# Kernel tuning notes

Hardware: AMD Instinct MI355X
Metric: run time of the kernel (lower is better)

Reference implementation:

```python
import jax, jax.numpy as jnp
import numpy as np

HIDDEN = 1024
NUM_HEADS = 8
HEAD_DIM = HIDDEN // NUM_HEADS
MAX_BACKWARD = 11   # context_left - 1
MAX_FORWARD = 12    # context_right
SPAN = MAX_BACKWARD + MAX_FORWARD + 1  # 24

B, U, W, C = 8, 16, 128, 151


def setup_inputs() -> dict:
    key = jax.random.key(0)
    kq, kk, kp = jax.random.split(key, 3)
    queries = jax.random.normal(kq, (B, U, W, NUM_HEADS, HEAD_DIM), dtype=jnp.float32)
    keys = jax.random.normal(kk, (B, U, C, NUM_HEADS, HEAD_DIM), dtype=jnp.float32)
    # glorot-ish scale for pos_proj (hidden, num_heads*head_dim)
    pos_proj = jax.random.normal(kp, (HIDDEN, NUM_HEADS * HEAD_DIM), dtype=jnp.float32) * (1.0 / np.sqrt(HIDDEN))
    return {"queries": queries, "keys": keys, "pos_proj": pos_proj}


def _sinusoid_emb(pos_proj):
    # positions: max_backward .. -max_forward (descending), shape (SPAN,)
    pos = jnp.arange(MAX_BACKWARD, -(MAX_FORWARD + 1), -1, dtype=jnp.float32)
    num_ts = HIDDEN // 2
    inv_ts = jnp.ones((num_ts,), dtype=jnp.float32)  # module uses ones
    scaled = pos[:, None] * inv_ts[None, :]          # (SPAN, HIDDEN/2)
    signal = jnp.concatenate([jnp.sin(scaled), jnp.cos(scaled)], axis=-1)  # (SPAN, HIDDEN)
    proj = signal @ pos_proj                         # (SPAN, N*H)
    return proj.reshape(SPAN, NUM_HEADS, HEAD_DIM)


def _relative_shift(term_bd, context_size):
    # term_bd: (B, N, U, W, SPAN) -> (B, N, U, W, C)
    b, n, u, w, _ = term_bd.shape
    pad = context_size + 1 - SPAN
    padded = jnp.pad(term_bd, ((0, 0), (0, 0), (0, 0), (0, 0), (0, pad)))
    flat = padded.reshape(b, n, u, w * (context_size + 1))
    sliced = flat[:, :, :, : w * context_size]
    return sliced.reshape(b, n, u, w, context_size)


def reference(queries, keys, pos_proj):
    context_size = keys.shape[2]
    sin_emb = _sinusoid_emb(pos_proj)                      # (SPAN, N, H)
    qp = jnp.transpose(queries, (0, 3, 1, 2, 4))           # (B, N, U, W, H)
    kp = jnp.transpose(keys, (0, 3, 1, 4, 2))              # (B, N, U, H, C)
    term_ac = jnp.matmul(qp, kp)                           # (B, N, U, W, C)
    # term_bd: query-position interaction, (B, N, U, W, SPAN)
    term_bd = jnp.einsum("bnuwh,fnh->bnuwf", qp, sin_emb)
    term_bd = _relative_shift(term_bd, context_size)       # (B, N, U, W, C)
    return term_ac + term_bd
```

## Files before the change

kernel.cpp:

```cpp
#include <hip/hip_runtime.h>
#include <cmath>

#define NHEADS 8
#define HDIM 128
#define SPAN 24
#define U_ 16
#define W_ 128
#define C_ 151
#define HID 1024

typedef unsigned short ushort8v __attribute__((ext_vector_type(8)));
typedef unsigned short ushort4v __attribute__((ext_vector_type(4)));
typedef __bf16 bf16x8 __attribute__((ext_vector_type(8)));
typedef float f32x4 __attribute__((ext_vector_type(4)));

__device__ inline unsigned short f2bf(float f) {
    union { float f; unsigned u; } v; v.f = f;
    unsigned r = v.u + 0x7FFFu + ((v.u >> 16) & 1u);
    return (unsigned short)(r >> 16);
}
__device__ inline float bf2f(unsigned short u) {
    union { unsigned u; float f; } v; v.u = ((unsigned)u) << 16;
    return v.f;
}
__device__ inline ushort8v cvt8(float4 a, float4 b) {
    ushort8v v;
    v[0] = f2bf(a.x); v[1] = f2bf(a.y); v[2] = f2bf(a.z); v[3] = f2bf(a.w);
    v[4] = f2bf(b.x); v[5] = f2bf(b.y); v[6] = f2bf(b.z); v[7] = f2bf(b.w);
    return v;
}

#define BAR() asm volatile("s_waitcnt lgkmcnt(0)\n\ts_barrier" ::: "memory")

__global__ void k_partial(const float* __restrict__ pp, float* __restrict__ part) {
    const int bi = blockIdx.x >> 2, cj = blockIdx.x & 3;
    const int col = cj * 256 + threadIdx.x * 4;
    const int row0 = bi * 16;
    float4 s = make_float4(0.f, 0.f, 0.f, 0.f);
    #pragma unroll
    for (int i = 0; i < 16; ++i) {
        float4 v = *(const float4*)(pp + (size_t)(row0 + i) * HID + col);
        s.x += v.x; s.y += v.y; s.z += v.z; s.w += v.w;
    }
    *(float4*)(part + (size_t)bi * HID + col) = s;
}

struct SC { float s[SPAN]; float c[SPAN]; };

#define CHUNK_B 8192
#define AUX_OFF 16384
#define S12_OFF (AUX_OFF + 4096)
#define BD_PITCH 25

__device__ inline ushort8v emb8(const char* lds_raw, int f, int u16, const SC& sc) {
    float4 s1a = *(const float4*)(lds_raw + S12_OFF + u16 * 32);
    float4 s1b = *(const float4*)(lds_raw + S12_OFF + u16 * 32 + 16);
    float4 s2a = *(const float4*)(lds_raw + S12_OFF + 512 + u16 * 32);
    float4 s2b = *(const float4*)(lds_raw + S12_OFF + 512 + u16 * 32 + 16);
    const float sf = sc.s[f], cf = sc.c[f];
    ushort8v v;
    v[0] = f2bf(sf * s1a.x + cf * s2a.x); v[1] = f2bf(sf * s1a.y + cf * s2a.y);
    v[2] = f2bf(sf * s1a.z + cf * s2a.z); v[3] = f2bf(sf * s1a.w + cf * s2a.w);
    v[4] = f2bf(sf * s1b.x + cf * s2b.x); v[5] = f2bf(sf * s1b.y + cf * s2b.y);
    v[6] = f2bf(sf * s1b.z + cf * s2b.z); v[7] = f2bf(sf * s1b.w + cf * s2b.w);
    return v;
}

#define ISSUE_K(c, P0, P1)                                                     \
    {                                                                          \
        const int r_ = 32 * (c) + (tid >> 4);                                  \
        if (r_ < C_) {                                                         \
            const float* s_ = k + kbase + (size_t)r_ * HID + u16 * 8;          \
            P0 = *(const float4*)s_; P1 = *(const float4*)(s_ + 4);            \
        }                                                                      \
    }

#define WRITE_PURE(P0, P1, BUFOFF)                                             \
    {                                                                          \
        const int rl_ = tid >> 4;                                              \
        const int dst_ = (BUFOFF) + rl_ * 256 + ((u16 * 16) ^ ((rl_ & 7) << 4));\
        *(ushort8v*)(lds_raw + dst_) = cvt8(P0, P1);                           \
    }

#define WRITE_C4(P0, P1, BUFOFF)                                               \
    {                                                                          \
        const int rl_ = tid >> 4;                                              \
        const int r_ = 128 + rl_;                                              \
        const int dst_ = (BUFOFF) + rl_ * 256 + ((u16 * 16) ^ ((rl_ & 7) << 4));\
        ushort8v v_;                                                           \
        if (r_ < C_) v_ = cvt8(P0, P1);                                        \
        else         v_ = emb8(lds_raw, r_ - C_, u16, sc);                     \
        *(ushort8v*)(lds_raw + dst_) = v_;                                     \
    }

#define WRITE_C5(BUFOFF)                                                       \
    if (tid < 256) {                                                           \
        const int rl_ = tid >> 4;                                              \
        const int r_ = 160 + rl_;                                              \
        const int dst_ = (BUFOFF) + rl_ * 256 + ((u16 * 16) ^ ((rl_ & 7) << 4));\
        ushort8v v_;                                                           \
        if (r_ < 175) v_ = emb8(lds_raw, r_ - C_, u16, sc);                    \
        else          v_ = (ushort8v)(unsigned short)0;                        \
        *(ushort8v*)(lds_raw + dst_) = v_;                                     \
    }

#define MFMA2(c, BUFOFF)                                                       \
    {                                                                          \
        _Pragma("unroll")                                                      \
        for (int kk = 0; kk < 4; ++kk) {                                       \
            _Pragma("unroll")                                                  \
            for (int jj = 0; jj < 2; ++jj) {                                   \
                const int rl = jj * 16 + lr;                                   \
                const int byt = (BUFOFF) + rl * 256 +                          \
                                (((kk * 64) + (lk * 16)) ^ ((rl & 7) << 4));   \
                bf16x8 bf = __builtin_bit_cast(bf16x8,                         \
                                *(const ushort8v*)(lds_raw + byt));            \
                acc[2 * (c) + jj] = __builtin_amdgcn_mfma_f32_16x16x32_bf16(   \
                                        qf[kk], bf, acc[2 * (c) + jj], 0, 0, 0);\
            }                                                                  \
        }                                                                      \
    }

#define MFMA1(BUFOFF)                                                          \
    {                                                                          \
        _Pragma("unroll")                                                      \
        for (int kk = 0; kk < 4; ++kk) {                                       \
            const int rl = lr;                                                 \
            const int byt = (BUFOFF) + rl * 256 +                              \
                            (((kk * 64) + (lk * 16)) ^ ((rl & 7) << 4));       \
            bf16x8 bf = __builtin_bit_cast(bf16x8,                             \
                            *(const ushort8v*)(lds_raw + byt));                \
            acc[10] = __builtin_amdgcn_mfma_f32_16x16x32_bf16(                 \
                          qf[kk], bf, acc[10], 0, 0, 0);                       \
        }                                                                      \
    }

#define STORE_TILE(J)                                                          \
    {                                                                          \
        const int c_ = (J) * 16 + lr;                                          \
        if (c_ < C_) {                                                         \
            _Pragma("unroll")                                                  \
            for (int reg = 0; reg < 4; ++reg) {                                \
                const int w_ = w0 + lk * 4 + reg;                              \
                float v_ = acc[J][reg];                                        \
                const int d_ = c_ - w_;                                        \
                if (d_ >= 0 && d_ < SPAN) v_ += bf2f(bd[w_ * BD_PITCH + d_]);  \
                out[obase + (size_t)w_ * C_ + c_] = v_;                        \
            }                                                                  \
        }                                                                      \
    }

__global__ __launch_bounds__(512, 4) void k_main(const float* __restrict__ q,
                                                 const float* __restrict__ k,
                                                 const float* __restrict__ part,
                                                 float* __restrict__ out, SC sc) {
    __shared__ __align__(16) char lds_raw[AUX_OFF + W_ * BD_PITCH * 2];
    unsigned short* bd = (unsigned short*)(lds_raw + AUX_OFF);

    const int bid = blockIdx.x;
    const int n = bid & 7;
    const int u = (bid >> 3) & 15;
    const int b = bid >> 7;

    const size_t qbase = ((size_t)(b * U_ + u) * W_) * HID + n * HDIM;
    const size_t kbase = ((size_t)(b * U_ + u) * C_) * HID + n * HDIM;
    const size_t obase = ((size_t)((b * NHEADS + n) * U_ + u)) * (W_ * C_);

    const int tid = threadIdx.x;
    const int lane = tid & 63;
    const int wave = tid >> 6;
    const int w0 = wave * 16;
    const int lr = lane & 15;
    const int lk = lane >> 4;
    const int u16 = tid & 15;

    const int c4 = tid & 31, rg = tid >> 5;
    float4 pp4[4];
    #pragma unroll
    for (int i = 0; i < 4; ++i)
        pp4[i] = *(const float4*)(part + (size_t)(rg * 4 + i) * HID + n * HDIM + c4 * 4);

    const float* qrow = q + qbase + (size_t)(w0 + lr) * HID + lk * 8;
    float4 qpf[8];
    #pragma unroll
    for (int kk = 0; kk < 4; ++kk) {
        qpf[2 * kk]     = *(const float4*)(qrow + kk * 32);
        qpf[2 * kk + 1] = *(const float4*)(qrow + kk * 32 + 4);
    }

    float4 a0, a1, b0, b1;
    ISSUE_K(4, a0, a1);
    ISSUE_K(0, b0, b1);

    {
        float4 rs;
        rs.x = pp4[0].x + pp4[1].x + pp4[2].x + pp4[3].x;
        rs.y = pp4[0].y + pp4[1].y + pp4[2].y + pp4[3].y;
        rs.z = pp4[0].z + pp4[1].z + pp4[2].z + pp4[3].z;
        rs.w = pp4[0].w + pp4[1].w + pp4[2].w + pp4[3].w;
        ushort4v rb;
        rb[0] = f2bf(rs.x); rb[1] = f2bf(rs.y); rb[2] = f2bf(rs.z); rb[3] = f2bf(rs.w);
        *(ushort4v*)(lds_raw + AUX_OFF + rg * 256 + c4 * 8) = rb;
    }
    BAR();

    if (tid < 256) {
        const int col = tid & 127, half = tid >> 7;
        float s = 0.f;
        #pragma unroll
        for (int g = 0; g < 8; ++g)
            s += bf2f(*(const unsigned short*)(lds_raw + AUX_OFF + (half * 8 + g) * 256 + col * 2));
        *(float*)(lds_raw + S12_OFF + (half * 128 + col) * 4) = s;
    }
    bf16x8 qf[4];
    #pragma unroll
    for (int kk = 0; kk < 4; ++kk)
        qf[kk] = __builtin_bit_cast(bf16x8, cvt8(qpf[2 * kk], qpf[2 * kk + 1]));

    f32x4 acc[11];
    #pragma unroll
    for (int j = 0; j < 11; ++j) acc[j] = (f32x4)(0.f);

    BAR();

    WRITE_C4(a0, a1, 0);
    BAR();

    MFMA2(4, 0);
    WRITE_C5(CHUNK_B);
    ISSUE_K(1, a0, a1);
    BAR();

    MFMA1(CHUNK_B);
    {
        const int c9 = 144 + lr;
        if (c9 >= C_) {
            const int f = c9 - C_;
            #pragma unroll
            for (int reg = 0; reg < 4; ++reg) {
                const int w = w0 + lk * 4 + reg;
                bd[w * BD_PITCH + f] = f2bf(acc[9][reg]);
            }
        }
        const int f10 = 9 + lr;
        if (f10 < SPAN) {
            #pragma unroll
            for (int reg = 0; reg < 4; ++reg) {
                const int w = w0 + lk * 4 + reg;
                bd[w * BD_PITCH + f10] = f2bf(acc[10][reg]);
            }
        }
    }
    WRITE_PURE(b0, b1, 0);
    ISSUE_K(2, b0, b1);
    BAR();

    MFMA2(0, 0);
    WRITE_PURE(a0, a1, CHUNK_B);
    ISSUE_K(3, a0, a1);
    STORE_TILE(8);
    STORE_TILE(9);
    BAR();

    MFMA2(1, CHUNK_B);
    WRITE_PURE(b0, b1, 0);
    STORE_TILE(0);
    STORE_TILE(1);
    BAR();

    MFMA2(2, 0);
    WRITE_PURE(a0, a1, CHUNK_B);
    STORE_TILE(2);
    STORE_TILE(3);
    BAR();

    MFMA2(3, CHUNK_B);
    STORE_TILE(4);
    STORE_TILE(5);

    STORE_TILE(6);
    STORE_TILE(7);
}

extern "C" void kernel_launch(void* const* d_in, const int* in_sizes, int n_in,
                              void* d_out, int out_size, void* d_ws, size_t ws_size,
                              hipStream_t stream) {
    const float* queries = (const float*)d_in[0];
    const float* keys    = (const float*)d_in[1];
    const float* posproj = (const float*)d_in[2];
    float* out = (float*)d_out;

    float* part = (float*)d_ws;

    SC sc;
    for (int f = 0; f < SPAN; ++f) {
        float p = (float)(11 - f);
        sc.s[f] = sinf(p);
        sc.c[f] = cosf(p);
    }

    k_partial<<<256, 64, 0, stream>>>(posproj, part);
    k_main<<<1024, 512, 0, stream>>>(queries, keys, part, out, sc);
}
```

Measured before the change: 49.43 us.

## Split each (b,u,n) block into two W-halves with 256-thread blocks

```diff
diff --git a/kernel.cpp b/kernel.cpp
--- a/kernel.cpp
+++ b/kernel.cpp
@@ -49,7 +49,7 @@
 
 #define CHUNK_B 8192
 #define AUX_OFF 16384
-#define S12_OFF (AUX_OFF + 4096)
+#define S12_OFF (AUX_OFF + 2048)
 #define BD_PITCH 25
 
 __device__ inline ushort8v emb8(const char* lds_raw, int f, int u16, const SC& sc) {
@@ -66,42 +66,50 @@
     return v;
 }
 
-#define ISSUE_K(c, P0, P1)                                                     \
-    {                                                                          \
-        const int r_ = 32 * (c) + (tid >> 4);                                  \
-        if (r_ < C_) {                                                         \
-            const float* s_ = k + kbase + (size_t)r_ * HID + u16 * 8;          \
-            P0 = *(const float4*)s_; P1 = *(const float4*)(s_ + 4);            \
-        }                                                                      \
-    }
-
-#define WRITE_PURE(P0, P1, BUFOFF)                                             \
-    {                                                                          \
-        const int rl_ = tid >> 4;                                              \
-        const int dst_ = (BUFOFF) + rl_ * 256 + ((u16 * 16) ^ ((rl_ & 7) << 4));\
-        *(ushort8v*)(lds_raw + dst_) = cvt8(P0, P1);                           \
-    }
-
-#define WRITE_C4(P0, P1, BUFOFF)                                               \
-    {                                                                          \
-        const int rl_ = tid >> 4;                                              \
-        const int r_ = 128 + rl_;                                              \
-        const int dst_ = (BUFOFF) + rl_ * 256 + ((u16 * 16) ^ ((rl_ & 7) << 4));\
+#define ISSUE_K(c, PA0, PA1, PB0, PB1)                                         \
+    {                                                                          \
+        const int rA_ = 32 * (c) + rl;                                         \
+        const int rB_ = rA_ + 16;                                              \
+        if (rA_ < C_) {                                                        \
+            const float* s_ = k + kbase + (size_t)rA_ * HID + u16 * 8;         \
+            PA0 = *(const float4*)s_; PA1 = *(const float4*)(s_ + 4);          \
+        }                                                                      \
+        if (rB_ < C_) {                                                        \
+            const float* s_ = k + kbase + (size_t)rB_ * HID + u16 * 8;         \
+            PB0 = *(const float4*)s_; PB1 = *(const float4*)(s_ + 4);          \
+        }                                                                      \
+    }
+
+#define WRITE_PURE(PA0, PA1, PB0, PB1, BUFOFF)                                 \
+    {                                                                          \
+        const int dA_ = (BUFOFF) + rl * 256 + ((u16 * 16) ^ ((rl & 7) << 4));  \
+        *(ushort8v*)(lds_raw + dA_) = cvt8(PA0, PA1);                          \
+        const int rB_ = rl + 16;                                               \
+        const int dB_ = (BUFOFF) + rB_ * 256 + ((u16 * 16) ^ ((rB_ & 7) << 4));\
+        *(ushort8v*)(lds_raw + dB_) = cvt8(PB0, PB1);                          \
+    }
+
+#define WRITE_C4(PA0, PA1, PB0, PB1, BUFOFF)                                   \
+    {                                                                          \
+        const int dA_ = (BUFOFF) + rl * 256 + ((u16 * 16) ^ ((rl & 7) << 4));  \
+        *(ushort8v*)(lds_raw + dA_) = cvt8(PA0, PA1);                          \
+        const int rB_ = rl + 16;                                               \
+        const int rG_ = 144 + rl;                                              \
+        const int dB_ = (BUFOFF) + rB_ * 256 + ((u16 * 16) ^ ((rB_ & 7) << 4));\
         ushort8v v_;                                                           \
-        if (r_ < C_) v_ = cvt8(P0, P1);                                        \
-        else         v_ = emb8(lds_raw, r_ - C_, u16, sc);                     \
-        *(ushort8v*)(lds_raw + dst_) = v_;                                     \
+        if (rG_ < C_) v_ = cvt8(PB0, PB1);                                     \
+        else          v_ = emb8(lds_raw, rG_ - C_, u16, sc);                   \
+        *(ushort8v*)(lds_raw + dB_) = v_;                                      \
     }
 
 #define WRITE_C5(BUFOFF)                                                       \
-    if (tid < 256) {                                                           \
-        const int rl_ = tid >> 4;                                              \
-        const int r_ = 160 + rl_;                                              \
-        const int dst_ = (BUFOFF) + rl_ * 256 + ((u16 * 16) ^ ((rl_ & 7) << 4));\
+    {                                                                          \
+        const int rG_ = 160 + rl;                                              \
+        const int d_ = (BUFOFF) + rl * 256 + ((u16 * 16) ^ ((rl & 7) << 4));   \
         ushort8v v_;                                                           \
-        if (r_ < 175) v_ = emb8(lds_raw, r_ - C_, u16, sc);                    \
-        else          v_ = (ushort8v)(unsigned short)0;                        \
-        *(ushort8v*)(lds_raw + dst_) = v_;                                     \
+        if (rG_ < 175) v_ = emb8(lds_raw, rG_ - C_, u16, sc);                  \
+        else           v_ = (ushort8v)(unsigned short)0;                       \
+        *(ushort8v*)(lds_raw + d_) = v_;                                       \
     }
 
 #define MFMA2(c, BUFOFF)                                                       \
@@ -110,9 +118,9 @@
         for (int kk = 0; kk < 4; ++kk) {                                       \
             _Pragma("unroll")                                                  \
             for (int jj = 0; jj < 2; ++jj) {                                   \
-                const int rl = jj * 16 + lr;                                   \
-                const int byt = (BUFOFF) + rl * 256 +                          \
-                                (((kk * 64) + (lk * 16)) ^ ((rl & 7) << 4));   \
+                const int rr = jj * 16 + lr;                                   \
+                const int byt = (BUFOFF) + rr * 256 +                          \
+                                (((kk * 64) + (lk * 16)) ^ ((rr & 7) << 4));   \
                 bf16x8 bf = __builtin_bit_cast(bf16x8,                         \
                                 *(const ushort8v*)(lds_raw + byt));            \
                 acc[2 * (c) + jj] = __builtin_amdgcn_mfma_f32_16x16x32_bf16(   \
@@ -125,9 +133,8 @@
     {                                                                          \
         _Pragma("unroll")                                                      \
         for (int kk = 0; kk < 4; ++kk) {                                       \
-            const int rl = lr;                                                 \
-            const int byt = (BUFOFF) + rl * 256 +                              \
-                            (((kk * 64) + (lk * 16)) ^ ((rl & 7) << 4));       \
+            const int byt = (BUFOFF) + lr * 256 +                              \
+                            (((kk * 64) + (lk * 16)) ^ ((lr & 7) << 4));       \
             bf16x8 bf = __builtin_bit_cast(bf16x8,                             \
                             *(const ushort8v*)(lds_raw + byt));                \
             acc[10] = __builtin_amdgcn_mfma_f32_16x16x32_bf16(                 \
@@ -142,25 +149,27 @@
             _Pragma("unroll")                                                  \
             for (int reg = 0; reg < 4; ++reg) {                                \
                 const int w_ = w0 + lk * 4 + reg;                              \
+                const int wg_ = hbase + w_;                                    \
                 float v_ = acc[J][reg];                                        \
-                const int d_ = c_ - w_;                                        \
+                const int d_ = c_ - wg_;                                       \
                 if (d_ >= 0 && d_ < SPAN) v_ += bf2f(bd[w_ * BD_PITCH + d_]);  \
-                out[obase + (size_t)w_ * C_ + c_] = v_;                        \
+                __builtin_nontemporal_store(v_, out + obase + (size_t)wg_ * C_ + c_); \
             }                                                                  \
         }                                                                      \
     }
 
-__global__ __launch_bounds__(512, 4) void k_main(const float* __restrict__ q,
+__global__ __launch_bounds__(256, 4) void k_main(const float* __restrict__ q,
                                                  const float* __restrict__ k,
                                                  const float* __restrict__ part,
                                                  float* __restrict__ out, SC sc) {
-    __shared__ __align__(16) char lds_raw[AUX_OFF + W_ * BD_PITCH * 2];
+    __shared__ __align__(16) char lds_raw[AUX_OFF + 3584];
     unsigned short* bd = (unsigned short*)(lds_raw + AUX_OFF);
 
     const int bid = blockIdx.x;
     const int n = bid & 7;
     const int u = (bid >> 3) & 15;
-    const int b = bid >> 7;
+    const int b = (bid >> 7) & 7;
+    const int hbase = (bid >> 10) * 64;
 
     const size_t qbase = ((size_t)(b * U_ + u) * W_) * HID + n * HDIM;
     const size_t kbase = ((size_t)(b * U_ + u) * C_) * HID + n * HDIM;
@@ -173,49 +182,49 @@
     const int lr = lane & 15;
     const int lk = lane >> 4;
     const int u16 = tid & 15;
+    const int rl = tid >> 4;
 
     const int c4 = tid & 31, rg = tid >> 5;
-    float4 pp4[4];
+    const float* pbase = part + n * HDIM + c4 * 4;
+    float4 ps0 = *(const float4*)(pbase + (size_t)(rg * 8 + 0) * HID);
+    float4 ps1 = *(const float4*)(pbase + (size_t)(rg * 8 + 1) * HID);
     #pragma unroll
-    for (int i = 0; i < 4; ++i)
-        pp4[i] = *(const float4*)(part + (size_t)(rg * 4 + i) * HID + n * HDIM + c4 * 4);
-
-    const float* qrow = q + qbase + (size_t)(w0 + lr) * HID + lk * 8;
-    float4 qpf[8];
+    for (int i = 2; i < 8; i += 2) {
+        float4 t0 = *(const float4*)(pbase + (size_t)(rg * 8 + i) * HID);
+        float4 t1 = *(const float4*)(pbase + (size_t)(rg * 8 + i + 1) * HID);
+        ps0.x += t0.x; ps0.y += t0.y; ps0.z += t0.z; ps0.w += t0.w;
+        ps1.x += t1.x; ps1.y += t1.y; ps1.z += t1.z; ps1.w += t1.w;
+    }
+
+    float4 a0, a1, a2, a3, b0, b1, b2, b3;
+    ISSUE_K(4, a0, a1, a2, a3);
+    ISSUE_K(0, b0, b1, b2, b3);
+
+    const float* qrow = q + qbase + (size_t)(hbase + w0 + lr) * HID + lk * 8;
+    bf16x8 qf[4];
     #pragma unroll
     for (int kk = 0; kk < 4; ++kk) {
-        qpf[2 * kk]     = *(const float4*)(qrow + kk * 32);
-        qpf[2 * kk + 1] = *(const float4*)(qrow + kk * 32 + 4);
-    }
-
-    float4 a0, a1, b0, b1;
-    ISSUE_K(4, a0, a1);
-    ISSUE_K(0, b0, b1);
+        float4 t0 = *(const float4*)(qrow + kk * 32);
+        float4 t1 = *(const float4*)(qrow + kk * 32 + 4);
+        qf[kk] = __builtin_bit_cast(bf16x8, cvt8(t0, t1));
+    }
 
     {
-        float4 rs;
-        rs.x = pp4[0].x + pp4[1].x + pp4[2].x + pp4[3].x;
-        rs.y = pp4[0].y + pp4[1].y + pp4[2].y + pp4[3].y;
-        rs.z = pp4[0].z + pp4[1].z + pp4[2].z + pp4[3].z;
-        rs.w = pp4[0].w + pp4[1].w + pp4[2].w + pp4[3].w;
+        ps0.x += ps1.x; ps0.y += ps1.y; ps0.z += ps1.z; ps0.w += ps1.w;
         ushort4v rb;
-        rb[0] = f2bf(rs.x); rb[1] = f2bf(rs.y); rb[2] = f2bf(rs.z); rb[3] = f2bf(rs.w);
+        rb[0] = f2bf(ps0.x); rb[1] = f2bf(ps0.y); rb[2] = f2bf(ps0.z); rb[3] = f2bf(ps0.w);
         *(ushort4v*)(lds_raw + AUX_OFF + rg * 256 + c4 * 8) = rb;
     }
     BAR();
 
-    if (tid < 256) {
-        const int col = tid & 127, half = tid >> 7;
+    {
+        const int col = tid & 127, hs = tid >> 7;
         float s = 0.f;
         #pragma unroll
-        for (int g = 0; g < 8; ++g)
-            s += bf2f(*(const unsigned short*)(lds_raw + AUX_OFF + (half * 8 + g) * 256 + col * 2));
-        *(float*)(lds_raw + S12_OFF + (half * 128 + col) * 4) = s;
-    }
-    bf16x8 qf[4];
-    #pragma unroll
-    for (int kk = 0; kk < 4; ++kk)
-        qf[kk] = __builtin_bit_cast(bf16x8, cvt8(qpf[2 * kk], qpf[2 * kk + 1]));
+        for (int g = 0; g < 4; ++g)
+            s += bf2f(*(const unsigned short*)(lds_raw + AUX_OFF + (hs * 4 + g) * 256 + col * 2));
+        *(float*)(lds_raw + S12_OFF + (hs * 128 + col) * 4) = s;
+    }
 
     f32x4 acc[11];
     #pragma unroll
@@ -223,12 +232,12 @@
 
     BAR();
 
-    WRITE_C4(a0, a1, 0);
+    WRITE_C4(a0, a1, a2, a3, 0);
     BAR();
 
     MFMA2(4, 0);
     WRITE_C5(CHUNK_B);
-    ISSUE_K(1, a0, a1);
+    ISSUE_K(1, a0, a1, a2, a3);
     BAR();
 
     MFMA1(CHUNK_B);
@@ -251,25 +260,25 @@
             }
         }
     }
-    WRITE_PURE(b0, b1, 0);
-    ISSUE_K(2, b0, b1);
+    WRITE_PURE(b0, b1, b2, b3, 0);
+    ISSUE_K(2, b0, b1, b2, b3);
     BAR();
 
     MFMA2(0, 0);
-    WRITE_PURE(a0, a1, CHUNK_B);
-    ISSUE_K(3, a0, a1);
+    WRITE_PURE(a0, a1, a2, a3, CHUNK_B);
+    ISSUE_K(3, a0, a1, a2, a3);
     STORE_TILE(8);
     STORE_TILE(9);
     BAR();
 
     MFMA2(1, CHUNK_B);
-    WRITE_PURE(b0, b1, 0);
+    WRITE_PURE(b0, b1, b2, b3, 0);
     STORE_TILE(0);
     STORE_TILE(1);
     BAR();
 
     MFMA2(2, 0);
-    WRITE_PURE(a0, a1, CHUNK_B);
+    WRITE_PURE(a0, a1, a2, a3, CHUNK_B);
     STORE_TILE(2);
     STORE_TILE(3);
     BAR();
@@ -277,7 +286,6 @@
     MFMA2(3, CHUNK_B);
     STORE_TILE(4);
     STORE_TILE(5);
-
     STORE_TILE(6);
     STORE_TILE(7);
 }
@@ -300,5 +308,5 @@
     }
 
     k_partial<<<256, 64, 0, stream>>>(posproj, part);
-    k_main<<<1024, 512, 0, stream>>>(queries, keys, part, out, sc);
-}
+    k_main<<<2048, 256, 0, stream>>>(queries, keys, part, out, sc);
+}
```

After: 97.63 us. +97.5%, slower.
